# Optimization experiments

Hardware: AMD Instinct MI355X
Metric: run time of the kernel (lower is better)

The kernel has to match this reference:

```python
import jax, jax.numpy as jnp
import numpy as np

N = 50_000          # num_nodes
E = 800_000         # num_edges (avg degree 16)
DIMS = [512, 256, 256, 7]   # embedding_dim
SCALING = 2.0


def _glorot(key, shape):
    lim = float(np.sqrt(6.0 / (shape[0] + shape[1])))
    return jax.random.uniform(key, shape, jnp.float32, -lim, lim)


def setup_inputs() -> dict:
    key = jax.random.key(0)
    ks = jax.random.split(key, 16)
    inp = {
        "x": jax.random.normal(ks[0], (N, DIMS[0]), jnp.float32),
        "edge_index": jax.random.randint(ks[1], (2, E), 0, N, dtype=jnp.int32),
        # GCNConv weights (3 layers)
        "W1": _glorot(ks[2], (DIMS[0], DIMS[1])), "b1": jnp.zeros((DIMS[1],), jnp.float32),
        "W2": _glorot(ks[3], (DIMS[1], DIMS[2])), "b2": jnp.zeros((DIMS[2],), jnp.float32),
        "W3": _glorot(ks[4], (DIMS[2], DIMS[3])), "b3": jnp.zeros((DIMS[3],), jnp.float32),
        # pseudo_mlp: Linear(512,512) -> ReLU -> Linear(512,64) -> ReLU -> Linear(64,out)
        "mw1": _glorot(ks[5], (DIMS[0], 512)), "mb1": jnp.zeros((512,), jnp.float32),
        "mw2": _glorot(ks[6], (512, 64)),      "mb2": jnp.zeros((64,), jnp.float32),
        "mw3": _glorot(ks[7], (64, DIMS[-1])), "mb3": jnp.zeros((DIMS[-1],), jnp.float32),
        # parsing_mats[0] (only index 0 is used: learn_soft_edge3 always called with ln=0)
        "parsing0": jnp.ones((DIMS[-1], DIMS[-1]), jnp.float32) / SCALING,
    }
    return inp


def _gcn_conv(h_in, row, col, edge_weight, W, b):
    """PyG-style GCNConv with self-loops, symmetric norm, and per-edge weights."""
    h = h_in @ W                                  # [N, out]
    loop = jnp.arange(N, dtype=row.dtype)
    r = jnp.concatenate([row, loop])
    c = jnp.concatenate([col, loop])
    ew = jnp.concatenate([edge_weight, jnp.ones((N,), h.dtype)])
    deg = jax.ops.segment_sum(ew, c, num_segments=N)
    dinv = jnp.where(deg > 0, jax.lax.rsqrt(jnp.maximum(deg, 1e-12)), 0.0)
    norm = dinv[r] * ew * dinv[c]                 # [E+N]
    out = jax.ops.segment_sum(h[r] * norm[:, None], c, num_segments=N)
    return out + b


def _learn_soft_edge(x, row, col, mw1, mb1, mw2, mb2, mw3, mb3, parsing0):
    # pseudo_mlp logits
    h = jax.nn.relu(x @ mw1 + mb1)
    h = jax.nn.relu(h @ mw2 + mb2)
    logits = h @ mw3 + mb3                        # [N, C]
    s = logits[row]                               # start_logits [E, C]
    e = logits[col]                               # end_logits   [E, C]
    parsing = jax.nn.relu(SCALING * parsing0)     # [C, C]
    # diag(bmm(outer(s,e), P)).sum(-1) == sum_{c,d} s[e,c] * e[e,d] * P[d,c]
    ew = jnp.sum(s * (e @ parsing), axis=1)       # [E]
    mean = ew.mean()
    var = ew.var(ddof=1)                          # torch .var() is unbiased
    return (ew - mean) * jnp.sqrt(1e-4 / var) + 1.0


def reference(x, edge_index, W1, b1, W2, b2, W3, b3,
              mw1, mb1, mw2, mb2, mw3, mb3, parsing0):
    row, col = edge_index[0], edge_index[1]
    ew = _learn_soft_edge(x, row, col, mw1, mb1, mw2, mb2, mw3, mb3, parsing0)
    # layer 0
    h0 = _gcn_conv(x, row, col, ew, W1, b1)       # h = x (saved, pre-ReLU)
    x1 = jax.nn.relu(h0)                          # dropout is identity in eval
    # layer 1 (+ residual to h0)
    x2 = _gcn_conv(x1, row, col, ew, W2, b2)
    x2 = jax.nn.relu(x2) + h0
    # layer 2 (final, no activation)
    out = _gcn_conv(x2, row, col, ew, W3, b3)     # [N, n_classes]
    return out
```

## Files before the change

### kernel.cpp

```cpp
#include <hip/hip_runtime.h>

#define NN 50000
#define EE 800000
#define NB_EDGE 3125
#define NB_SCAN 196

typedef __attribute__((ext_vector_type(4))) float f32x4;
typedef __attribute__((ext_vector_type(8))) short bf16x8;
typedef __attribute__((ext_vector_type(8))) unsigned short u16x8;

typedef const __attribute__((address_space(1))) void* gas_p;
typedef __attribute__((address_space(3))) void* las_p;

__device__ __forceinline__ float bf2f(unsigned short u) {
  union { unsigned int i; float f; } v; v.i = ((unsigned int)u) << 16; return v.f;
}
__device__ __forceinline__ unsigned short f2bf(float f) {
  union { float f; unsigned int i; } v; v.f = f;
  unsigned int u = v.i;
  return (unsigned short)((u + 0x7FFFu + ((u >> 16) & 1u)) >> 16);
}

__device__ __forceinline__ int xcd_swizzle(int orig, int nwg) {
  int xcd = orig & 7;
  int pos = orig >> 3;
  int q = nwg >> 3, r = nwg & 7;
  return (xcd < r ? xcd * (q + 1) : r * (q + 1) + (xcd - r) * q) + pos;
}

constexpr size_t O_XBF  = 0;
constexpr size_t O_H1   = O_XBF + 51200000;
constexpr size_t O_G1   = O_H1  + 51200000;
constexpr size_t O_X1   = O_G1  + 25600000;
constexpr size_t O_H2   = O_X1  + 25600000;
constexpr size_t O_LG   = O_H2  + 6400000;
constexpr size_t O_TG   = O_LG  + 1600000;
constexpr size_t O_EWR  = O_TG  + 1600000;
constexpr size_t O_EWS  = O_EWR + 3200000;
constexpr size_t O_CSR  = O_EWS + 3200000;
constexpr size_t O_MW1T = O_CSR + 6400000;
constexpr size_t O_W1T  = O_MW1T + 524288;
constexpr size_t O_W2T  = O_W1T  + 262144;
constexpr size_t O_MW2T = O_W2T  + 131072;
constexpr size_t O_DEG  = O_MW2T + 65536;
constexpr size_t O_CNT  = O_DEG  + 200192;
constexpr size_t O_CUR  = O_CNT  + 200192;
constexpr size_t O_RED  = O_CUR  + 200192;
constexpr size_t O_RPT  = O_RED  + 256;
constexpr size_t O_DINV = O_RPT  + 200192;
constexpr size_t O_BSUM = O_DINV + 200192;

__global__ __launch_bounds__(256) void conv_f2bf4(const float* __restrict__ in,
                                                  unsigned short* __restrict__ out, int n4) {
  int i = blockIdx.x * 256 + threadIdx.x;
  if (i >= n4) return;
  const float4 v = ((const float4*)in)[i];
  ushort4 o; o.x = f2bf(v.x); o.y = f2bf(v.y); o.z = f2bf(v.z); o.w = f2bf(v.w);
  ((ushort4*)out)[i] = o;
}

__global__ __launch_bounds__(256)
void conv_weights(const float* __restrict__ mw1, const float* __restrict__ W1,
                  const float* __restrict__ W2, const float* __restrict__ mw2,
                  unsigned short* __restrict__ mw1t, unsigned short* __restrict__ w1t,
                  unsigned short* __restrict__ w2t, unsigned short* __restrict__ mw2t)
{
  int i = blockIdx.x * 256 + threadIdx.x;
  if (i < 262144) {
    int k = i >> 9, n = i & 511;
    mw1t[(size_t)n * 512 + k] = f2bf(mw1[i]);
  } else if (i < 393216) {
    int j = i - 262144, k = j >> 8, n = j & 255;
    w1t[(size_t)n * 512 + k] = f2bf(W1[j]);
  } else if (i < 458752) {
    int j = i - 393216, k = j >> 8, n = j & 255;
    w2t[(size_t)n * 256 + k] = f2bf(W2[j]);
  } else if (i < 491520) {
    int j = i - 458752, k = j >> 6, n = j & 63;
    mw2t[(size_t)n * 512 + k] = f2bf(mw2[j]);
  }
}

#define GEMM_STAGE(buf, k0)                                                        \
  _Pragma("unroll")                                                                \
  for (int r = 0; r < 4; ++r) {                                                    \
    const int row = r * 32 + wid * 8 + srow8;                                      \
    int ga = bm + row; ga = ga < M_ ? ga : M_ - 1;                                 \
    int gb = bn + row; gb = gb < N_ ? gb : N_ - 1;                                 \
    __builtin_amdgcn_global_load_lds((gas_p)(pA_ + ((size_t)ga * lda_ + (k0)) * 2 + sks * 16), \
                                     (las_p)(ldsA[buf] + row * 64), 16, 0, 0);     \
    __builtin_amdgcn_global_load_lds((gas_p)(pB_ + ((size_t)gb * ldb_ + (k0)) * 2 + sks * 16), \
                                     (las_p)(ldsB[buf] + row * 64), 16, 0, 0);     \
  }

#define GEMM_BODY(A, lda, Bt, ldb_K, M, Ncols, K, bm, bn)                          \
  __shared__ unsigned short ldsA[2][128 * 64];                                     \
  __shared__ unsigned short ldsB[2][128 * 64];                                     \
  const char* pA_ = (const char*)(A);                                              \
  const char* pB_ = (const char*)(Bt);                                             \
  const int lda_ = (lda), ldb_ = (ldb_K), M_ = (M), N_ = (Ncols);                  \
  const int tid  = threadIdx.x;                                                    \
  const int lane = tid & 63;                                                       \
  const int wid  = tid >> 6;                                                       \
  const int wm   = (wid >> 1) << 6;                                                \
  const int wn   = (wid & 1) << 6;                                                 \
  f32x4 acc[4][4] = {};                                                            \
  const int srow8 = lane >> 3;                                                     \
  const int sks   = (lane & 7) ^ srow8;                                            \
  const int nt    = (K) >> 6;                                                      \
  GEMM_STAGE(0, 0)                                                                 \
  for (int t = 0; t < nt; ++t) {                                                   \
    const int cur = t & 1;                                                         \
    if (t + 1 < nt) {                                                              \
      GEMM_STAGE(cur ^ 1, (t + 1) << 6)                                            \
      asm volatile("s_waitcnt vmcnt(8)" ::: "memory");                             \
    } else {                                                                       \
      asm volatile("s_waitcnt vmcnt(0)" ::: "memory");                             \
    }                                                                              \
    __builtin_amdgcn_s_barrier();                                                  \
    __builtin_amdgcn_sched_barrier(0);                                             \
    const int q   = lane >> 4;                                                     \
    const int r15 = lane & 15;                                                     \
    _Pragma("unroll")                                                              \
    for (int kk = 0; kk < 2; ++kk) {                                               \
      bf16x8 af[4], bfr[4];                                                        \
      _Pragma("unroll")                                                            \
      for (int m = 0; m < 4; ++m) {                                                \
        const int ra = wm + m * 16 + r15;                                          \
        af[m]  = *(const bf16x8*)(ldsA[cur] + ra * 64 + (((kk << 2) + q) ^ (ra & 7)) * 8); \
        const int rb = wn + m * 16 + r15;                                          \
        bfr[m] = *(const bf16x8*)(ldsB[cur] + rb * 64 + (((kk << 2) + q) ^ (rb & 7)) * 8); \
      }                                                                            \
      _Pragma("unroll")                                                            \
      for (int m = 0; m < 4; ++m)                                                  \
        _Pragma("unroll")                                                          \
        for (int n = 0; n < 4; ++n)                                                \
          acc[m][n] = __builtin_amdgcn_mfma_f32_16x16x32_bf16(af[m], bfr[n], acc[m][n], 0, 0, 0); \
    }                                                                              \
    __builtin_amdgcn_sched_barrier(0);                                             \
    __builtin_amdgcn_s_barrier();                                                  \
  }

template<bool RELU, bool BIAS>
__global__ __launch_bounds__(256)
void gemm_bf16(const unsigned short* __restrict__ A, int lda,
               const unsigned short* __restrict__ Bt,
               const float* __restrict__ bias,
               unsigned short* __restrict__ C, int ldc,
               int M, int N, int K)
{
  const int nwg  = gridDim.x * gridDim.y;
  const int wgid = xcd_swizzle(blockIdx.y * gridDim.x + blockIdx.x, nwg);
  const int bn   = (wgid % gridDim.x) << 7;
  const int bm   = (wgid / gridDim.x) << 7;

  GEMM_BODY(A, lda, Bt, K, M, N, K, bm, bn)

  const int q   = lane >> 4;
  const int r15 = lane & 15;
#pragma unroll
  for (int m = 0; m < 4; ++m) {
#pragma unroll
    for (int n = 0; n < 4; ++n) {
      const int gc = bn + wn + n * 16 + r15;
#pragma unroll
      for (int i = 0; i < 4; ++i) {
        const int gr = bm + wm + m * 16 + q * 4 + i;
        if (gr < M && gc < N) {
          float f = acc[m][n][i];
          if (BIAS) f += bias[gc];
          if (RELU) f = fmaxf(f, 0.f);
          C[(size_t)gr * ldc + gc] = f2bf(f);
        }
      }
    }
  }
}

__global__ __launch_bounds__(256)
void gemm_fused(const unsigned short* __restrict__ A,
                const unsigned short* __restrict__ Bt,
                const float* __restrict__ mb1,
                unsigned short* __restrict__ h1,
                unsigned short* __restrict__ g1,
                int M)
{
  const int nwg  = gridDim.x * gridDim.y;
  const int wgid = xcd_swizzle(blockIdx.y * gridDim.x + blockIdx.x, nwg);
  const int bnt  = wgid % gridDim.x;
  const int bn   = bnt << 7;
  const int bm   = (wgid / gridDim.x) << 7;

  GEMM_BODY(A, 512, Bt, 512, M, 768, 512, bm, bn)

  const int q   = lane >> 4;
  const int r15 = lane & 15;
  if (bnt < 4) {
#pragma unroll
    for (int m = 0; m < 4; ++m) {
#pragma unroll
      for (int n = 0; n < 4; ++n) {
        const int gc = bn + wn + n * 16 + r15;
        const float b = mb1[gc];
#pragma unroll
        for (int i = 0; i < 4; ++i) {
          const int gr = bm + wm + m * 16 + q * 4 + i;
          if (gr < M) h1[(size_t)gr * 512 + gc] = f2bf(fmaxf(acc[m][n][i] + b, 0.f));
        }
      }
    }
  } else {
#pragma unroll
    for (int m = 0; m < 4; ++m) {
#pragma unroll
      for (int n = 0; n < 4; ++n) {
        const int gc = bn - 512 + wn + n * 16 + r15;
#pragma unroll
        for (int i = 0; i < 4; ++i) {
          const int gr = bm + wm + m * 16 + q * 4 + i;
          if (gr < M) g1[(size_t)gr * 256 + gc] = f2bf(acc[m][n][i]);
        }
      }
    }
  }
}

__global__ __launch_bounds__(256)
void logits_kernel(const unsigned short* __restrict__ h2, const float* __restrict__ mw3,
                   const float* __restrict__ mb3, const float* __restrict__ par,
                   float* __restrict__ Lg, float* __restrict__ Tg)
{
  __shared__ float w[64 * 8];
  __shared__ float P[64];
  int tid = threadIdx.x;
  for (int i = tid; i < 512; i += 256) {
    int k = i >> 3, c = i & 7;
    w[i] = (c < 7) ? mw3[k * 7 + c] : 0.f;
  }
  if (tid < 64) {
    int d = tid >> 3, c = tid & 7;
    P[tid] = (d < 7 && c < 7) ? fmaxf(2.0f * par[d * 7 + c], 0.f) : 0.f;
  }
  __syncthreads();
  int n = blockIdx.x * 256 + tid;
  if (n >= NN) return;
  const unsigned short* hr = h2 + (size_t)n * 64;
  f32x4 L0 = {0,0,0,0}, L1 = {0,0,0,0};
  for (int k = 0; k < 64; k += 4) {
    ushort4 v = *(const ushort4*)(hr + k);
    float xs[4] = {bf2f(v.x), bf2f(v.y), bf2f(v.z), bf2f(v.w)};
#pragma unroll
    for (int j = 0; j < 4; ++j) {
      L0 += xs[j] * *(const f32x4*)&w[(k + j) * 8];
      L1 += xs[j] * *(const f32x4*)&w[(k + j) * 8 + 4];
    }
  }
  float Ls[8] = {L0[0], L0[1], L0[2], L0[3], L1[0], L1[1], L1[2], 0.f};
#pragma unroll
  for (int c = 0; c < 7; ++c) Ls[c] += mb3[c];
  f32x4 T0 = {0,0,0,0}, T1 = {0,0,0,0};
#pragma unroll
  for (int d = 0; d < 7; ++d) {
    T0 += Ls[d] * *(const f32x4*)&P[d * 8];
    T1 += Ls[d] * *(const f32x4*)&P[d * 8 + 4];
  }
  f32x4 o0 = {Ls[0], Ls[1], Ls[2], Ls[3]};
  f32x4 o1 = {Ls[4], Ls[5], Ls[6], 0.f};
  *(f32x4*)(Lg + (size_t)n * 8)     = o0;
  *(f32x4*)(Lg + (size_t)n * 8 + 4) = o1;
  *(f32x4*)(Tg + (size_t)n * 8)     = T0;
  *(f32x4*)(Tg + (size_t)n * 8 + 4) = T1;
}

__global__ __launch_bounds__(256)
void edge1_kernel(const int* __restrict__ row, const int* __restrict__ col,
                  const float* __restrict__ Lg, const float* __restrict__ Tg,
                  float* __restrict__ ew_raw, int* __restrict__ cnt,
                  double* __restrict__ part)
{
  __shared__ double shs[4], shs2[4];
  int e = blockIdx.x * 256 + threadIdx.x;
  double s = 0.0, s2 = 0.0;
  if (e < EE) {
    int r = row[e], c = col[e];
    float4 a0 = *(const float4*)(Lg + (size_t)r * 8);
    float4 a1 = *(const float4*)(Lg + (size_t)r * 8 + 4);
    float4 b0 = *(const float4*)(Tg + (size_t)c * 8);
    float4 b1 = *(const float4*)(Tg + (size_t)c * 8 + 4);
    float v = a0.x*b0.x + a0.y*b0.y + a0.z*b0.z + a0.w*b0.w
            + a1.x*b1.x + a1.y*b1.y + a1.z*b1.z + a1.w*b1.w;
    ew_raw[e] = v;
    atomicAdd(&cnt[c], 1);
    s = (double)v; s2 = (double)v * (double)v;
  }
  for (int off = 32; off; off >>= 1) {
    s  += __shfl_down(s, off);
    s2 += __shfl_down(s2, off);
  }
  int wv = threadIdx.x >> 6;
  if ((threadIdx.x & 63) == 0) { shs[wv] = s; shs2[wv] = s2; }
  __syncthreads();
  if (threadIdx.x == 0) {
    part[blockIdx.x]           = shs[0] + shs[1] + shs[2] + shs[3];
    part[NB_EDGE + blockIdx.x] = shs2[0] + shs2[1] + shs2[2] + shs2[3];
  }
}

__global__ __launch_bounds__(1024)
void redpart_kernel(const double* __restrict__ part, double* __restrict__ red)
{
  __shared__ double sh[16][2];
  int tid = threadIdx.x;
  double s = 0.0, s2 = 0.0;
  for (int i = tid; i < NB_EDGE; i += 1024) {
    s  += part[i];
    s2 += part[NB_EDGE + i];
  }
  for (int off = 32; off; off >>= 1) {
    s  += __shfl_down(s, off);
    s2 += __shfl_down(s2, off);
  }
  if ((tid & 63) == 0) { sh[tid >> 6][0] = s; sh[tid >> 6][1] = s2; }
  __syncthreads();
  if (tid == 0) {
    double a = 0.0, b = 0.0;
    for (int i = 0; i < 16; ++i) { a += sh[i][0]; b += sh[i][1]; }
    red[0] = a; red[1] = b;
  }
}

__global__ __launch_bounds__(256)
void edge2_kernel(const float* __restrict__ ew_raw, const int* __restrict__ col,
                  const double* __restrict__ red,
                  float* __restrict__ ew_std, float* __restrict__ deg)
{
  int e = blockIdx.x * 256 + threadIdx.x;
  if (e >= EE) return;
  double mean = red[0] / (double)EE;
  double var  = (red[1] - (double)EE * mean * mean) / (double)(EE - 1);
  double scl  = sqrt(1e-4 / var);
  float v = (float)(((double)ew_raw[e] - mean) * scl) + 1.0f;
  ew_std[e] = v;
  atomicAdd(&deg[col[e]], v);
}

__global__ __launch_bounds__(256)
void dinv_kernel(const float* __restrict__ deg, float* __restrict__ dinv)
{
  int n = blockIdx.x * 256 + threadIdx.x;
  if (n >= NN) return;
  float d = deg[n] + 1.0f;
  dinv[n] = d > 0.f ? 1.0f / sqrtf(fmaxf(d, 1e-12f)) : 0.f;
}

__global__ __launch_bounds__(256)
void scan1_kernel(const int* __restrict__ cnt, int* __restrict__ bsum)
{
  __shared__ int sh[4];
  int i = blockIdx.x * 256 + threadIdx.x;
  int v = (i < NN) ? cnt[i] : 0;
  for (int off = 32; off; off >>= 1) v += __shfl_down(v, off);
  if ((threadIdx.x & 63) == 0) sh[threadIdx.x >> 6] = v;
  __syncthreads();
  if (threadIdx.x == 0) bsum[blockIdx.x] = sh[0] + sh[1] + sh[2] + sh[3];
}

__global__ __launch_bounds__(256)
void scan2_kernel(int* __restrict__ bsum)
{
  __shared__ int sh[256];
  int tid = threadIdx.x;
  int v = (tid < NB_SCAN) ? bsum[tid] : 0;
  sh[tid] = v;
  __syncthreads();
  for (int off = 1; off < 256; off <<= 1) {
    int t = (tid >= off) ? sh[tid - off] : 0;
    __syncthreads();
    sh[tid] += t;
    __syncthreads();
  }
  if (tid < NB_SCAN) bsum[tid] = sh[tid] - v;
}

__global__ __launch_bounds__(256)
void scan3_kernel(const int* __restrict__ cnt, const int* __restrict__ bsum,
                  int* __restrict__ rowptr)
{
  __shared__ int sh[256];
  int tid = threadIdx.x;
  int i = blockIdx.x * 256 + tid;
  int v = (i < NN) ? cnt[i] : 0;
  sh[tid] = v;
  __syncthreads();
  for (int off = 1; off < 256; off <<= 1) {
    int t = (tid >= off) ? sh[tid - off] : 0;
    __syncthreads();
    sh[tid] += t;
    __syncthreads();
  }
  if (i < NN) rowptr[i + 1] = bsum[blockIdx.x] + sh[tid];
  if (i == 0) rowptr[0] = 0;
}

__global__ __launch_bounds__(256)
void edge3_kernel(const int* __restrict__ row, const int* __restrict__ col,
                  const float* __restrict__ ew_std, const float* __restrict__ dinv,
                  const int* __restrict__ rowptr, int* __restrict__ cursor,
                  int2* __restrict__ csr_sw)
{
  int e = blockIdx.x * 256 + threadIdx.x;
  if (e >= EE) return;
  int r = row[e], c = col[e];
  float w = dinv[r] * ew_std[e] * dinv[c];
  int pos = atomicAdd(&cursor[c], 1);
  int2 sw; sw.x = r; sw.y = __float_as_int(w);
  csr_sw[rowptr[c] + pos] = sw;
}

#define AGG_ACC(sw_, v_)                                                     \
  {                                                                          \
    float w_ = __int_as_float((sw_).y);                                      \
    a0 += w_ * bf2f((v_)[0]); a1 += w_ * bf2f((v_)[1]);                      \
    a2 += w_ * bf2f((v_)[2]); a3 += w_ * bf2f((v_)[3]);                      \
    a4 += w_ * bf2f((v_)[4]); a5 += w_ * bf2f((v_)[5]);                      \
    a6 += w_ * bf2f((v_)[6]); a7 += w_ * bf2f((v_)[7]);                      \
  }

template<int MODE>
__global__ __launch_bounds__(256)
void agg256_kernel(const int* __restrict__ rowptr, const int2* __restrict__ csr_sw,
                   const unsigned short* __restrict__ gsrc,
                   const float* __restrict__ dinv, const float* __restrict__ bias,
                   const unsigned short* __restrict__ h0in,
                   unsigned short* __restrict__ h0out,
                   unsigned short* __restrict__ xout)
{
  int n = blockIdx.x * 4 + (threadIdx.x >> 6);
  if (n >= NN) return;
  const int lane = threadIdx.x & 63;
  const int half = lane >> 5;
  const int l5   = lane & 31;
  const size_t colbase = (size_t)(l5 << 3);

  float a0=0,a1=0,a2=0,a3=0,a4=0,a5=0,a6=0,a7=0;
  const int s = rowptr[n], e = rowptr[n + 1];
  int i = s + half;
  for (; i + 14 < e; i += 16) {
    int2 sw[8];
#pragma unroll
    for (int u = 0; u < 8; ++u) sw[u] = csr_sw[i + 2 * u];
    u16x8 v[8];
#pragma unroll
    for (int u = 0; u < 8; ++u) v[u] = *(const u16x8*)(gsrc + (size_t)sw[u].x * 256 + colbase);
#pragma unroll
    for (int u = 0; u < 8; ++u) AGG_ACC(sw[u], v[u])
  }
  for (; i + 6 < e; i += 8) {
    int2 sw[4];
#pragma unroll
    for (int u = 0; u < 4; ++u) sw[u] = csr_sw[i + 2 * u];
    u16x8 v[4];
#pragma unroll
    for (int u = 0; u < 4; ++u) v[u] = *(const u16x8*)(gsrc + (size_t)sw[u].x * 256 + colbase);
#pragma unroll
    for (int u = 0; u < 4; ++u) AGG_ACC(sw[u], v[u])
  }
  for (; i < e; i += 2) {
    int2 sw = csr_sw[i];
    u16x8 v = *(const u16x8*)(gsrc + (size_t)sw.x * 256 + colbase);
    AGG_ACC(sw, v)
  }
  a0 += __shfl_xor(a0, 32); a1 += __shfl_xor(a1, 32);
  a2 += __shfl_xor(a2, 32); a3 += __shfl_xor(a3, 32);
  a4 += __shfl_xor(a4, 32); a5 += __shfl_xor(a5, 32);
  a6 += __shfl_xor(a6, 32); a7 += __shfl_xor(a7, 32);
  float f0 = half ? a4 : a0;
  float f1 = half ? a5 : a1;
  float f2 = half ? a6 : a2;
  float f3 = half ? a7 : a3;
  const int dbase = (l5 << 3) + (half << 2);
  float wd = dinv[n]; wd *= wd;
  ushort4 sv = *(const ushort4*)(gsrc + (size_t)n * 256 + dbase);
  f0 += wd * bf2f(sv.x); f1 += wd * bf2f(sv.y);
  f2 += wd * bf2f(sv.z); f3 += wd * bf2f(sv.w);
  float4 b = *(const float4*)(bias + dbase);
  f0 += b.x; f1 += b.y; f2 += b.z; f3 += b.w;
  const size_t o = (size_t)n * 256 + dbase;
  if (MODE == 0) {
    ushort4 h;
    h.x = f2bf(f0); h.y = f2bf(f1); h.z = f2bf(f2); h.w = f2bf(f3);
    *(ushort4*)(h0out + o) = h;
    ushort4 xo;
    xo.x = f2bf(fmaxf(f0, 0.f)); xo.y = f2bf(fmaxf(f1, 0.f));
    xo.z = f2bf(fmaxf(f2, 0.f)); xo.w = f2bf(fmaxf(f3, 0.f));
    *(ushort4*)(xout + o) = xo;
  } else {
    ushort4 h = *(const ushort4*)(h0in + o);
    ushort4 xo;
    xo.x = f2bf(fmaxf(f0, 0.f) + bf2f(h.x));
    xo.y = f2bf(fmaxf(f1, 0.f) + bf2f(h.y));
    xo.z = f2bf(fmaxf(f2, 0.f) + bf2f(h.z));
    xo.w = f2bf(fmaxf(f3, 0.f) + bf2f(h.w));
    *(ushort4*)(xout + o) = xo;
  }
}

__global__ __launch_bounds__(256)
void gemv7_kernel(const unsigned short* __restrict__ x2, const float* __restrict__ W3,
                  float* __restrict__ y3)
{
  __shared__ float w[256 * 8];
  int tid = threadIdx.x;
  for (int i = tid; i < 2048; i += 256) {
    int k = i >> 3, c = i & 7;
    w[i] = (c < 7) ? W3[k * 7 + c] : 0.f;
  }
  __syncthreads();
  int n = blockIdx.x * 256 + tid;
  if (n >= NN) return;
  const unsigned short* xr = x2 + (size_t)n * 256;
  f32x4 accLo = {0,0,0,0}, accHi = {0,0,0,0};
  for (int k = 0; k < 256; k += 4) {
    ushort4 v = *(const ushort4*)(xr + k);
    float xs[4] = {bf2f(v.x), bf2f(v.y), bf2f(v.z), bf2f(v.w)};
#pragma unroll
    for (int j = 0; j < 4; ++j) {
      accLo += xs[j] * *(const f32x4*)&w[(k + j) * 8];
      accHi += xs[j] * *(const f32x4*)&w[(k + j) * 8 + 4];
    }
  }
  *(f32x4*)(y3 + (size_t)n * 8)     = accLo;
  *(f32x4*)(y3 + (size_t)n * 8 + 4) = accHi;
}

__global__ __launch_bounds__(256)
void agg7_kernel(const int* __restrict__ rowptr, const int2* __restrict__ csr_sw,
                 const float* __restrict__ y3,
                 const float* __restrict__ dinv, const float* __restrict__ b3,
                 float* __restrict__ out)
{
  int n = blockIdx.x * 32 + (threadIdx.x >> 3);
  if (n >= NN) return;
  int j = threadIdx.x & 7;
  float acc = 0.f;
  int s = rowptr[n], e = rowptr[n + 1];
  for (int i = s; i < e; ++i) {
    int2 sw = csr_sw[i];
    acc += __int_as_float(sw.y) * y3[(size_t)sw.x * 8 + j];
  }
  float wd = dinv[n]; wd *= wd;
  acc += wd * y3[(size_t)n * 8 + j];
  if (j < 7) out[(size_t)n * 7 + j] = acc + b3[j];
}

extern "C" void kernel_launch(void* const* d_in, const int* in_sizes, int n_in,
                              void* d_out, int out_size, void* d_ws, size_t ws_size,
                              hipStream_t stream)
{
  const float* x   = (const float*)d_in[0];
  const int*   ei  = (const int*)d_in[1];
  const float* W1  = (const float*)d_in[2];
  const float* b1  = (const float*)d_in[3];
  const float* W2  = (const float*)d_in[4];
  const float* b2  = (const float*)d_in[5];
  const float* W3  = (const float*)d_in[6];
  const float* b3  = (const float*)d_in[7];
  const float* mw1 = (const float*)d_in[8];
  const float* mb1 = (const float*)d_in[9];
  const float* mw2 = (const float*)d_in[10];
  const float* mb2 = (const float*)d_in[11];
  const float* mw3 = (const float*)d_in[12];
  const float* mb3 = (const float*)d_in[13];
  const float* par = (const float*)d_in[14];
  const int* row = ei;
  const int* col = ei + EE;
  float* out = (float*)d_out;

  char* ws = (char*)d_ws;
  unsigned short* x_bf  = (unsigned short*)(ws + O_XBF);
  unsigned short* h0    = (unsigned short*)(ws + O_XBF);
  unsigned short* h1_bf = (unsigned short*)(ws + O_H1);
  unsigned short* g2_bf = (unsigned short*)(ws + O_H1);
  unsigned short* x2_bf = (unsigned short*)(ws + O_H1 + 25600000);
  unsigned short* g1_bf = (unsigned short*)(ws + O_G1);
  unsigned short* x1_bf = (unsigned short*)(ws + O_X1);
  unsigned short* h2_bf = (unsigned short*)(ws + O_H2);
  float* Lg      = (float*)(ws + O_LG);
  float* Tg      = (float*)(ws + O_TG);
  float* ew_raw  = (float*)(ws + O_EWR);
  float* y3      = (float*)(ws + O_EWR);
  float* ew_std  = (float*)(ws + O_EWS);
  int2*  csr_sw  = (int2*)(ws + O_CSR);
  double* part   = (double*)(ws + O_CSR);
  unsigned short* mw1t = (unsigned short*)(ws + O_MW1T);
  unsigned short* w1t  = (unsigned short*)(ws + O_W1T);
  unsigned short* w2t  = (unsigned short*)(ws + O_W2T);
  unsigned short* mw2t = (unsigned short*)(ws + O_MW2T);
  float*  deg    = (float*)(ws + O_DEG);
  int*    cnt    = (int*)(ws + O_CNT);
  int*    cursor = (int*)(ws + O_CUR);
  double* red    = (double*)(ws + O_RED);
  int*    rowptr = (int*)(ws + O_RPT);
  float*  dinv   = (float*)(ws + O_DINV);
  int*    bsum   = (int*)(ws + O_BSUM);

  hipMemsetAsync(ws + O_DEG, 0, 3 * 200192, stream);

  conv_f2bf4<<<25000, 256, 0, stream>>>(x, x_bf, NN * 512 / 4);
  conv_weights<<<1920, 256, 0, stream>>>(mw1, W1, W2, mw2, mw1t, w1t, w2t, mw2t);

  gemm_fused<<<dim3(6, 391), 256, 0, stream>>>(x_bf, mw1t, mb1, h1_bf, g1_bf, NN);
  gemm_bf16<true,  true ><<<dim3(1, 391), 256, 0, stream>>>(h1_bf, 512, mw2t, mb2, h2_bf, 64, NN, 64, 512);
  logits_kernel<<<196, 256, 0, stream>>>(h2_bf, mw3, mb3, par, Lg, Tg);

  edge1_kernel<<<NB_EDGE, 256, 0, stream>>>(row, col, Lg, Tg, ew_raw, cnt, part);
  redpart_kernel<<<1, 1024, 0, stream>>>(part, red);
  edge2_kernel<<<NB_EDGE, 256, 0, stream>>>(ew_raw, col, red, ew_std, deg);
  dinv_kernel<<<196, 256, 0, stream>>>(deg, dinv);
  scan1_kernel<<<NB_SCAN, 256, 0, stream>>>(cnt, bsum);
  scan2_kernel<<<1, 256, 0, stream>>>(bsum);
  scan3_kernel<<<NB_SCAN, 256, 0, stream>>>(cnt, bsum, rowptr);
  edge3_kernel<<<NB_EDGE, 256, 0, stream>>>(row, col, ew_std, dinv, rowptr, cursor, csr_sw);

  agg256_kernel<0><<<12500, 256, 0, stream>>>(rowptr, csr_sw, g1_bf, dinv, b1, nullptr, h0, x1_bf);
  gemm_bf16<false, false><<<dim3(2, 391), 256, 0, stream>>>(x1_bf, 256, w2t, nullptr, g2_bf, 256, NN, 256, 256);
  agg256_kernel<1><<<12500, 256, 0, stream>>>(rowptr, csr_sw, g2_bf, dinv, b2, h0, nullptr, x2_bf);
  gemv7_kernel<<<196, 256, 0, stream>>>(x2_bf, W3, y3);
  agg7_kernel<<<1563, 256, 0, stream>>>(rowptr, csr_sw, y3, dinv, b3, out);
}
```

Baseline: 453.3 us.

## Fuse edge normalization into CSR build, fold gemv7 into layer-2 aggregation

Merges edge2 and edge3 into one kernel that standardizes edge weights and scatters them straight into the CSR, so dinv is no longer needed before the CSR is built. The dinv[src] factor is now applied inside the aggregation loops and dinv[dst] in the epilogue. The 256-to-7 projection (gemv7) is fused into the MODE-1 aggregation through per-wave shuffle reductions, which removes the x2 buffer round trip. edge1 now processes two edges per thread and the 16-wide unrolled aggregation loop is dropped. The cost is an extra dinv gather per edge in every aggregation and a full-wave shuffle reduction per node.

After: 462.7 us. 2.1% more time.

```diff
diff --git a/kernel.cpp b/kernel.cpp
--- a/kernel.cpp
+++ b/kernel.cpp
@@ -3,6 +3,7 @@
 #define NN 50000
 #define EE 800000
 #define NB_EDGE 3125
+#define NB_E1   1563
 #define NB_SCAN 196
 
 typedef __attribute__((ext_vector_type(4))) float f32x4;
@@ -279,19 +280,39 @@
                   double* __restrict__ part)
 {
   __shared__ double shs[4], shs2[4];
-  int e = blockIdx.x * 256 + threadIdx.x;
+  const int e0 = blockIdx.x * 512 + threadIdx.x;
+  const int e1 = e0 + 256;
   double s = 0.0, s2 = 0.0;
-  if (e < EE) {
-    int r = row[e], c = col[e];
-    float4 a0 = *(const float4*)(Lg + (size_t)r * 8);
-    float4 a1 = *(const float4*)(Lg + (size_t)r * 8 + 4);
-    float4 b0 = *(const float4*)(Tg + (size_t)c * 8);
-    float4 b1 = *(const float4*)(Tg + (size_t)c * 8 + 4);
-    float v = a0.x*b0.x + a0.y*b0.y + a0.z*b0.z + a0.w*b0.w
-            + a1.x*b1.x + a1.y*b1.y + a1.z*b1.z + a1.w*b1.w;
-    ew_raw[e] = v;
-    atomicAdd(&cnt[c], 1);
-    s = (double)v; s2 = (double)v * (double)v;
+  if (e1 < EE) {
+    int r0 = row[e0], c0 = col[e0];
+    int r1 = row[e1], c1 = col[e1];
+    float4 a00 = *(const float4*)(Lg + (size_t)r0 * 8);
+    float4 a01 = *(const float4*)(Lg + (size_t)r0 * 8 + 4);
+    float4 a10 = *(const float4*)(Lg + (size_t)r1 * 8);
+    float4 a11 = *(const float4*)(Lg + (size_t)r1 * 8 + 4);
+    float4 b00 = *(const float4*)(Tg + (size_t)c0 * 8);
+    float4 b01 = *(const float4*)(Tg + (size_t)c0 * 8 + 4);
+    float4 b10 = *(const float4*)(Tg + (size_t)c1 * 8);
+    float4 b11 = *(const float4*)(Tg + (size_t)c1 * 8 + 4);
+    float v0 = a00.x*b00.x + a00.y*b00.y + a00.z*b00.z + a00.w*b00.w
+             + a01.x*b01.x + a01.y*b01.y + a01.z*b01.z + a01.w*b01.w;
+    float v1 = a10.x*b10.x + a10.y*b10.y + a10.z*b10.z + a10.w*b10.w
+             + a11.x*b11.x + a11.y*b11.y + a11.z*b11.z + a11.w*b11.w;
+    ew_raw[e0] = v0; ew_raw[e1] = v1;
+    atomicAdd(&cnt[c0], 1); atomicAdd(&cnt[c1], 1);
+    s = (double)v0 + (double)v1;
+    s2 = (double)v0 * (double)v0 + (double)v1 * (double)v1;
+  } else if (e0 < EE) {
+    int r0 = row[e0], c0 = col[e0];
+    float4 a00 = *(const float4*)(Lg + (size_t)r0 * 8);
+    float4 a01 = *(const float4*)(Lg + (size_t)r0 * 8 + 4);
+    float4 b00 = *(const float4*)(Tg + (size_t)c0 * 8);
+    float4 b01 = *(const float4*)(Tg + (size_t)c0 * 8 + 4);
+    float v0 = a00.x*b00.x + a00.y*b00.y + a00.z*b00.z + a00.w*b00.w
+             + a01.x*b01.x + a01.y*b01.y + a01.z*b01.z + a01.w*b01.w;
+    ew_raw[e0] = v0;
+    atomicAdd(&cnt[c0], 1);
+    s = (double)v0; s2 = (double)v0 * (double)v0;
   }
   for (int off = 32; off; off >>= 1) {
     s  += __shfl_down(s, off);
@@ -301,8 +322,8 @@
   if ((threadIdx.x & 63) == 0) { shs[wv] = s; shs2[wv] = s2; }
   __syncthreads();
   if (threadIdx.x == 0) {
-    part[blockIdx.x]           = shs[0] + shs[1] + shs[2] + shs[3];
-    part[NB_EDGE + blockIdx.x] = shs2[0] + shs2[1] + shs2[2] + shs2[3];
+    part[blockIdx.x]         = shs[0] + shs[1] + shs[2] + shs[3];
+    part[NB_E1 + blockIdx.x] = shs2[0] + shs2[1] + shs2[2] + shs2[3];
   }
 }
 
@@ -312,9 +333,9 @@
   __shared__ double sh[16][2];
   int tid = threadIdx.x;
   double s = 0.0, s2 = 0.0;
-  for (int i = tid; i < NB_EDGE; i += 1024) {
+  for (int i = tid; i < NB_E1; i += 1024) {
     s  += part[i];
-    s2 += part[NB_EDGE + i];
+    s2 += part[NB_E1 + i];
   }
   for (int off = 32; off; off >>= 1) {
     s  += __shfl_down(s, off);
@@ -330,9 +351,10 @@
 }
 
 __global__ __launch_bounds__(256)
-void edge2_kernel(const float* __restrict__ ew_raw, const int* __restrict__ col,
-                  const double* __restrict__ red,
-                  float* __restrict__ ew_std, float* __restrict__ deg)
+void edge2_kernel(const int* __restrict__ row, const int* __restrict__ col,
+                  const float* __restrict__ ew_raw, const double* __restrict__ red,
+                  const int* __restrict__ rowptr, int* __restrict__ cursor,
+                  float* __restrict__ deg, int2* __restrict__ csr_sw)
 {
   int e = blockIdx.x * 256 + threadIdx.x;
   if (e >= EE) return;
@@ -340,8 +362,11 @@
   double var  = (red[1] - (double)EE * mean * mean) / (double)(EE - 1);
   double scl  = sqrt(1e-4 / var);
   float v = (float)(((double)ew_raw[e] - mean) * scl) + 1.0f;
-  ew_std[e] = v;
-  atomicAdd(&deg[col[e]], v);
+  int c = col[e];
+  atomicAdd(&deg[c], v);
+  int pos = atomicAdd(&cursor[c], 1);
+  int2 sw; sw.x = row[e]; sw.y = __float_as_int(v);
+  csr_sw[rowptr[c] + pos] = sw;
 }
 
 __global__ __launch_bounds__(256)
@@ -402,24 +427,9 @@
   if (i == 0) rowptr[0] = 0;
 }
 
-__global__ __launch_bounds__(256)
-void edge3_kernel(const int* __restrict__ row, const int* __restrict__ col,
-                  const float* __restrict__ ew_std, const float* __restrict__ dinv,
-                  const int* __restrict__ rowptr, int* __restrict__ cursor,
-                  int2* __restrict__ csr_sw)
-{
-  int e = blockIdx.x * 256 + threadIdx.x;
-  if (e >= EE) return;
-  int r = row[e], c = col[e];
-  float w = dinv[r] * ew_std[e] * dinv[c];
-  int pos = atomicAdd(&cursor[c], 1);
-  int2 sw; sw.x = r; sw.y = __float_as_int(w);
-  csr_sw[rowptr[c] + pos] = sw;
-}
-
-#define AGG_ACC(sw_, v_)                                                     \
+#define AGG_ACC(sw_, v_, dv_)                                                \
   {                                                                          \
-    float w_ = __int_as_float((sw_).y);                                      \
+    float w_ = __int_as_float((sw_).y) * (dv_);                              \
     a0 += w_ * bf2f((v_)[0]); a1 += w_ * bf2f((v_)[1]);                      \
     a2 += w_ * bf2f((v_)[2]); a3 += w_ * bf2f((v_)[3]);                      \
     a4 += w_ * bf2f((v_)[4]); a5 += w_ * bf2f((v_)[5]);                      \
@@ -433,8 +443,17 @@
                    const float* __restrict__ dinv, const float* __restrict__ bias,
                    const unsigned short* __restrict__ h0in,
                    unsigned short* __restrict__ h0out,
-                   unsigned short* __restrict__ xout)
-{
+                   unsigned short* __restrict__ xout,
+                   const float* __restrict__ W3, float* __restrict__ y3)
+{
+  __shared__ float wlds[2048];
+  if (MODE == 1) {
+    for (int i = threadIdx.x; i < 2048; i += 256) {
+      int c = i & 7;
+      wlds[i] = (c < 7) ? W3[(i >> 3) * 7 + c] : 0.f;
+    }
+    __syncthreads();
+  }
   int n = blockIdx.x * 4 + (threadIdx.x >> 6);
   if (n >= NN) return;
   const int lane = threadIdx.x & 63;
@@ -445,30 +464,25 @@
   float a0=0,a1=0,a2=0,a3=0,a4=0,a5=0,a6=0,a7=0;
   const int s = rowptr[n], e = rowptr[n + 1];
   int i = s + half;
-  for (; i + 14 < e; i += 16) {
-    int2 sw[8];
-#pragma unroll
-    for (int u = 0; u < 8; ++u) sw[u] = csr_sw[i + 2 * u];
-    u16x8 v[8];
-#pragma unroll
-    for (int u = 0; u < 8; ++u) v[u] = *(const u16x8*)(gsrc + (size_t)sw[u].x * 256 + colbase);
-#pragma unroll
-    for (int u = 0; u < 8; ++u) AGG_ACC(sw[u], v[u])
-  }
   for (; i + 6 < e; i += 8) {
     int2 sw[4];
 #pragma unroll
     for (int u = 0; u < 4; ++u) sw[u] = csr_sw[i + 2 * u];
+    float dv[4];
     u16x8 v[4];
 #pragma unroll
-    for (int u = 0; u < 4; ++u) v[u] = *(const u16x8*)(gsrc + (size_t)sw[u].x * 256 + colbase);
-#pragma unroll
-    for (int u = 0; u < 4; ++u) AGG_ACC(sw[u], v[u])
+    for (int u = 0; u < 4; ++u) {
+      dv[u] = dinv[sw[u].x];
+      v[u]  = *(const u16x8*)(gsrc + (size_t)sw[u].x * 256 + colbase);
+    }
+#pragma unroll
+    for (int u = 0; u < 4; ++u) AGG_ACC(sw[u], v[u], dv[u])
   }
   for (; i < e; i += 2) {
     int2 sw = csr_sw[i];
+    float dv = dinv[sw.x];
     u16x8 v = *(const u16x8*)(gsrc + (size_t)sw.x * 256 + colbase);
-    AGG_ACC(sw, v)
+    AGG_ACC(sw, v, dv)
   }
   a0 += __shfl_xor(a0, 32); a1 += __shfl_xor(a1, 32);
   a2 += __shfl_xor(a2, 32); a3 += __shfl_xor(a3, 32);
@@ -479,12 +493,14 @@
   float f2 = half ? a6 : a2;
   float f3 = half ? a7 : a3;
   const int dbase = (l5 << 3) + (half << 2);
-  float wd = dinv[n]; wd *= wd;
+  const float dn = dinv[n];
+  const float wd = dn * dn;
   ushort4 sv = *(const ushort4*)(gsrc + (size_t)n * 256 + dbase);
-  f0 += wd * bf2f(sv.x); f1 += wd * bf2f(sv.y);
-  f2 += wd * bf2f(sv.z); f3 += wd * bf2f(sv.w);
   float4 b = *(const float4*)(bias + dbase);
-  f0 += b.x; f1 += b.y; f2 += b.z; f3 += b.w;
+  f0 = dn * f0 + wd * bf2f(sv.x) + b.x;
+  f1 = dn * f1 + wd * bf2f(sv.y) + b.y;
+  f2 = dn * f2 + wd * bf2f(sv.z) + b.z;
+  f3 = dn * f3 + wd * bf2f(sv.w) + b.w;
   const size_t o = (size_t)n * 256 + dbase;
   if (MODE == 0) {
     ushort4 h;
@@ -496,41 +512,31 @@
     *(ushort4*)(xout + o) = xo;
   } else {
     ushort4 h = *(const ushort4*)(h0in + o);
-    ushort4 xo;
-    xo.x = f2bf(fmaxf(f0, 0.f) + bf2f(h.x));
-    xo.y = f2bf(fmaxf(f1, 0.f) + bf2f(h.y));
-    xo.z = f2bf(fmaxf(f2, 0.f) + bf2f(h.z));
-    xo.w = f2bf(fmaxf(f3, 0.f) + bf2f(h.w));
-    *(ushort4*)(xout + o) = xo;
-  }
-}
-
-__global__ __launch_bounds__(256)
-void gemv7_kernel(const unsigned short* __restrict__ x2, const float* __restrict__ W3,
-                  float* __restrict__ y3)
-{
-  __shared__ float w[256 * 8];
-  int tid = threadIdx.x;
-  for (int i = tid; i < 2048; i += 256) {
-    int k = i >> 3, c = i & 7;
-    w[i] = (c < 7) ? W3[k * 7 + c] : 0.f;
-  }
-  __syncthreads();
-  int n = blockIdx.x * 256 + tid;
-  if (n >= NN) return;
-  const unsigned short* xr = x2 + (size_t)n * 256;
-  f32x4 accLo = {0,0,0,0}, accHi = {0,0,0,0};
-  for (int k = 0; k < 256; k += 4) {
-    ushort4 v = *(const ushort4*)(xr + k);
-    float xs[4] = {bf2f(v.x), bf2f(v.y), bf2f(v.z), bf2f(v.w)};
-#pragma unroll
-    for (int j = 0; j < 4; ++j) {
-      accLo += xs[j] * *(const f32x4*)&w[(k + j) * 8];
-      accHi += xs[j] * *(const f32x4*)&w[(k + j) * 8 + 4];
-    }
-  }
-  *(f32x4*)(y3 + (size_t)n * 8)     = accLo;
-  *(f32x4*)(y3 + (size_t)n * 8 + 4) = accHi;
+    float x0 = bf2f(f2bf(fmaxf(f0, 0.f) + bf2f(h.x)));
+    float x1 = bf2f(f2bf(fmaxf(f1, 0.f) + bf2f(h.y)));
+    float x2v = bf2f(f2bf(fmaxf(f2, 0.f) + bf2f(h.z)));
+    float x3 = bf2f(f2bf(fmaxf(f3, 0.f) + bf2f(h.w)));
+    f32x4 p0 = {0,0,0,0}, p1 = {0,0,0,0};
+    p0 += x0 * *(const f32x4*)&wlds[(dbase + 0) * 8];
+    p1 += x0 * *(const f32x4*)&wlds[(dbase + 0) * 8 + 4];
+    p0 += x1 * *(const f32x4*)&wlds[(dbase + 1) * 8];
+    p1 += x1 * *(const f32x4*)&wlds[(dbase + 1) * 8 + 4];
+    p0 += x2v * *(const f32x4*)&wlds[(dbase + 2) * 8];
+    p1 += x2v * *(const f32x4*)&wlds[(dbase + 2) * 8 + 4];
+    p0 += x3 * *(const f32x4*)&wlds[(dbase + 3) * 8];
+    p1 += x3 * *(const f32x4*)&wlds[(dbase + 3) * 8 + 4];
+#pragma unroll
+    for (int off = 1; off < 64; off <<= 1) {
+      p0[0] += __shfl_xor(p0[0], off); p0[1] += __shfl_xor(p0[1], off);
+      p0[2] += __shfl_xor(p0[2], off); p0[3] += __shfl_xor(p0[3], off);
+      p1[0] += __shfl_xor(p1[0], off); p1[1] += __shfl_xor(p1[1], off);
+      p1[2] += __shfl_xor(p1[2], off); p1[3] += __shfl_xor(p1[3], off);
+    }
+    if (lane == 0) {
+      *(f32x4*)(y3 + (size_t)n * 8)     = p0;
+      *(f32x4*)(y3 + (size_t)n * 8 + 4) = p1;
+    }
+  }
 }
 
 __global__ __launch_bounds__(256)
@@ -546,10 +552,10 @@
   int s = rowptr[n], e = rowptr[n + 1];
   for (int i = s; i < e; ++i) {
     int2 sw = csr_sw[i];
-    acc += __int_as_float(sw.y) * y3[(size_t)sw.x * 8 + j];
-  }
-  float wd = dinv[n]; wd *= wd;
-  acc += wd * y3[(size_t)n * 8 + j];
+    acc += __int_as_float(sw.y) * dinv[sw.x] * y3[(size_t)sw.x * 8 + j];
+  }
+  float dn = dinv[n];
+  acc = dn * acc + dn * dn * y3[(size_t)n * 8 + j];
   if (j < 7) out[(size_t)n * 7 + j] = acc + b3[j];
 }
 
@@ -581,7 +587,6 @@
   unsigned short* h0    = (unsigned short*)(ws + O_XBF);
   unsigned short* h1_bf = (unsigned short*)(ws + O_H1);
   unsigned short* g2_bf = (unsigned short*)(ws + O_H1);
-  unsigned short* x2_bf = (unsigned short*)(ws + O_H1 + 25600000);
   unsigned short* g1_bf = (unsigned short*)(ws + O_G1);
   unsigned short* x1_bf = (unsigned short*)(ws + O_X1);
   unsigned short* h2_bf = (unsigned short*)(ws + O_H2);
@@ -589,7 +594,6 @@
   float* Tg      = (float*)(ws + O_TG);
   float* ew_raw  = (float*)(ws + O_EWR);
   float* y3      = (float*)(ws + O_EWR);
-  float* ew_std  = (float*)(ws + O_EWS);
   int2*  csr_sw  = (int2*)(ws + O_CSR);
   double* part   = (double*)(ws + O_CSR);
   unsigned short* mw1t = (unsigned short*)(ws + O_MW1T);
@@ -613,18 +617,16 @@
   gemm_bf16<true,  true ><<<dim3(1, 391), 256, 0, stream>>>(h1_bf, 512, mw2t, mb2, h2_bf, 64, NN, 64, 512);
   logits_kernel<<<196, 256, 0, stream>>>(h2_bf, mw3, mb3, par, Lg, Tg);
 
-  edge1_kernel<<<NB_EDGE, 256, 0, stream>>>(row, col, Lg, Tg, ew_raw, cnt, part);
+  edge1_kernel<<<NB_E1, 256, 0, stream>>>(row, col, Lg, Tg, ew_raw, cnt, part);
   redpart_kernel<<<1, 1024, 0, stream>>>(part, red);
-  edge2_kernel<<<NB_EDGE, 256, 0, stream>>>(ew_raw, col, red, ew_std, deg);
-  dinv_kernel<<<196, 256, 0, stream>>>(deg, dinv);
   scan1_kernel<<<NB_SCAN, 256, 0, stream>>>(cnt, bsum);
   scan2_kernel<<<1, 256, 0, stream>>>(bsum);
   scan3_kernel<<<NB_SCAN, 256, 0, stream>>>(cnt, bsum, rowptr);
-  edge3_kernel<<<NB_EDGE, 256, 0, stream>>>(row, col, ew_std, dinv, rowptr, cursor, csr_sw);
-
-  agg256_kernel<0><<<12500, 256, 0, stream>>>(rowptr, csr_sw, g1_bf, dinv, b1, nullptr, h0, x1_bf);
+  edge2_kernel<<<NB_EDGE, 256, 0, stream>>>(row, col, ew_raw, red, rowptr, cursor, deg, csr_sw);
+  dinv_kernel<<<196, 256, 0, stream>>>(deg, dinv);
+
+  agg256_kernel<0><<<12500, 256, 0, stream>>>(rowptr, csr_sw, g1_bf, dinv, b1, nullptr, h0, x1_bf, nullptr, nullptr);
   gemm_bf16<false, false><<<dim3(2, 391), 256, 0, stream>>>(x1_bf, 256, w2t, nullptr, g2_bf, 256, NN, 256, 256);
-  agg256_kernel<1><<<12500, 256, 0, stream>>>(rowptr, csr_sw, g2_bf, dinv, b2, h0, nullptr, x2_bf);
-  gemv7_kernel<<<196, 256, 0, stream>>>(x2_bf, W3, y3);
+  agg256_kernel<1><<<12500, 256, 0, stream>>>(rowptr, csr_sw, g2_bf, dinv, b2, h0, nullptr, nullptr, W3, y3);
   agg7_kernel<<<1563, 256, 0, stream>>>(rowptr, csr_sw, y3, dinv, b3, out);
 }
```
